# Kernel tuning notes

Hardware: AMD Instinct MI355X
Metric: run time of the kernel (lower is better)

The kernel has to match this reference:

```python
import jax, jax.numpy as jnp
import numpy as np

VX, VY = 0.2, 0.2
X_OFF = VX / 2 + 0.0          # vx/2 + pc_range[0]
Y_OFF = VY / 2 + (-40.0)      # vy/2 + pc_range[1]
K = 8                          # hardcoded in GCNLayer
BN_EPS = 1e-3
LRELU_SLOPE = 0.2
V, T, C_IN, C_OUT = 4096, 100, 4, 64


def _gcn_layer(x, conv_w, bn_gamma, bn_beta, bn_mean, bn_var):
    """DGCNN EdgeConv layer. x: [N, T, C]. Returns [N, T, O]."""
    N, Tn, C = x.shape
    # KNN on negative squared distance (self included in topk, as in torch code)
    xx = jnp.sum(x * x, axis=-1)                       # [N, T]
    inner = jnp.einsum('ntc,nsc->nts', x, x)           # [N, T, T]
    neg_dist = 2.0 * inner - xx[:, :, None] - xx[:, None, :]
    _, idx = jax.lax.top_k(neg_dist, K)                # [N, T, K]
    # gather neighbor features: nbr[n,t,k,c] = x[n, idx[n,t,k], c]
    nbr = x[jnp.arange(N)[:, None, None], idx]         # [N, T, K, C]
    xc = x[:, :, None, :]                              # [N, T, 1, C]
    edge = jnp.concatenate(
        [nbr - xc, jnp.broadcast_to(xc, (N, Tn, K, C))], axis=-1)  # [N,T,K,2C]
    # 1x1 conv (no bias) + eval-mode BatchNorm + LeakyReLU(0.2)
    h = jnp.einsum('ntkc,oc->ntko', edge, conv_w)      # [N, T, K, O]
    scale = bn_gamma / jnp.sqrt(bn_var + BN_EPS)
    h = (h - bn_mean) * scale + bn_beta
    h = jax.nn.leaky_relu(h, LRELU_SLOPE)
    return jnp.max(h, axis=2)                          # max over k -> [N, T, O]


def setup_inputs() -> dict:
    key = jax.random.key(0)
    k1, k2, k3, k4, k5, k6 = jax.random.split(key, 6)
    features = jax.random.normal(k1, (V, T, C_IN), dtype=jnp.float32)
    num_voxels = jnp.maximum(
        jax.random.randint(k2, (V,), 0, T), 1).astype(jnp.int32)
    coors = jax.random.randint(k3, (V, 4), 0, 352).astype(jnp.int32)
    # GCNLayer params: Conv2d(18, 64, 1, bias=False) + BatchNorm2d(64)
    conv_w = jax.random.normal(k4, (C_OUT, 18), dtype=jnp.float32) * 0.1
    bn_gamma = jnp.ones((C_OUT,), jnp.float32)
    bn_beta = jnp.zeros((C_OUT,), jnp.float32)
    bn_mean = jax.random.normal(k5, (C_OUT,), jnp.float32) * 0.1
    bn_var = 1.0 + 0.1 * jax.random.uniform(k6, (C_OUT,), jnp.float32)
    return {"features": features, "conv_w": conv_w, "bn_gamma": bn_gamma,
            "bn_beta": bn_beta, "bn_mean": bn_mean, "bn_var": bn_var,
            "num_voxels": num_voxels, "coors": coors}


def reference(features, conv_w, bn_gamma, bn_beta, bn_mean, bn_var,
              num_voxels, coors):
    nv = num_voxels.astype(features.dtype)
    # decorate: cluster offsets (xyz - mean) and pillar-center offsets (xy)
    points_mean = jnp.sum(features[:, :, :3], axis=1, keepdims=True) / nv[:, None, None]
    f_cluster = features[:, :, :3] - points_mean                      # [V,T,3]
    fx = features[:, :, 0] - (coors[:, 3].astype(features.dtype)[:, None] * VX + X_OFF)
    fy = features[:, :, 1] - (coors[:, 2].astype(features.dtype)[:, None] * VY + Y_OFF)
    f_center = jnp.stack([fx, fy], axis=-1)                           # [V,T,2]
    feat = jnp.concatenate([features, f_cluster, f_center], axis=-1)  # [V,T,9]
    # padding mask: point t valid iff t < num_voxels[v]
    mask = (jnp.arange(T)[None, :] < num_voxels[:, None]).astype(features.dtype)
    feat = feat * mask[:, :, None]
    # single GCN (last) layer; batch_process chunking is a no-op mathematically
    out = _gcn_layer(feat, conv_w, bn_gamma, bn_beta, bn_mean, bn_var)  # [V,T,64]
    out = out * mask[:, :, None]            # (+ zeros prev_features_out)
    out = jnp.max(out, axis=1)              # max over points -> [V, 64]
    return out
```

## Files before the change

kernel.cpp:

```cpp
#include <hip/hip_runtime.h>

#define TPTS 100
#define CO   64
#define KK   8

__device__ __forceinline__ unsigned umin_(unsigned a, unsigned b) { return a < b ? a : b; }
__device__ __forceinline__ unsigned umax_(unsigned a, unsigned b) { return a > b ? a : b; }

__device__ __forceinline__ unsigned dist_key(const float4 qt, const float4 qs, unsigned s) {
    float dx = qt.x - qs.x, dy = qt.y - qs.y;
    float dz = qt.z - qs.z, dw = qt.w - qs.w;
    float e = __fmaf_rn(dx, dx, __fmaf_rn(dy, dy, __fmaf_rn(dz, dz, dw * dw)));
    return (__float_as_uint(e) & 0xFFFFFF80u) | s;
}

__device__ __forceinline__ void ins8(unsigned val[KK], unsigned key) {
    #pragma unroll
    for (int k = KK - 1; k >= 1; --k)
        val[k] = umin_(val[k], umax_(val[k - 1], key));
    val[0] = umin_(val[0], key);
}

__global__ __launch_bounds__(256) void dgcnn_kernel(
    const float* __restrict__ features,
    const float* __restrict__ conv_w,
    const float* __restrict__ bn_gamma,
    const float* __restrict__ bn_beta,
    const float* __restrict__ bn_mean,
    const float* __restrict__ bn_var,
    const int*  __restrict__ num_voxels,
    const int*  __restrict__ coors,
    float* __restrict__ out)
{
    __shared__ float    s_feat[TPTS][12];
    __shared__ float    s_xx[TPTS];
    __shared__ unsigned s_idxp[TPTS][2];
    __shared__ float    s_red[4][CO];
    __shared__ float    s_mean[4];
    __shared__ union {
        float stage[TPTS][4];
        float g[TPTS][CO];
    } s_u;

    const float INF = __builtin_inff();
    const int v   = blockIdx.x;
    const int tid = threadIdx.x;
    const int nv  = num_voxels[v];

    float4 f = make_float4(0.f, 0.f, 0.f, 0.f);
    if (tid < TPTS) {
        f = reinterpret_cast<const float4*>(features)[v * TPTS + tid];
        *reinterpret_cast<float4*>(&s_u.stage[tid][0]) = f;
    }
    __syncthreads();

    if (tid < 96) {
        int ch = tid >> 5, j = tid & 31;
        float p = s_u.stage[j][ch] + s_u.stage[j + 32][ch] + s_u.stage[j + 64][ch];
        if (j < 4) p += s_u.stage[j + 96][ch];
        #pragma unroll
        for (int off = 16; off >= 1; off >>= 1)
            p += __shfl_xor(p, off, 32);
        if (j == 0) s_mean[ch] = p / (float)nv;
    }
    __syncthreads();

    if (tid < TPTS) {
        float mask = (tid < nv) ? 1.0f : 0.0f;
        float c3 = (float)coors[v * 4 + 3];
        float c2 = (float)coors[v * 4 + 2];
        float r0 = f.x * mask, r1 = f.y * mask, r2 = f.z * mask, r3 = f.w * mask;
        float r4 = (f.x - s_mean[0]) * mask;
        float r5 = (f.y - s_mean[1]) * mask;
        float r6 = (f.z - s_mean[2]) * mask;
        float r7 = (f.x - (c3 * 0.2f + 0.1f)) * mask;
        float r8 = (f.y - (c2 * 0.2f - 39.9f)) * mask;
        float xx = r0*r0 + r1*r1 + r2*r2 + r3*r3 + r4*r4
                 + r5*r5 + r6*r6 + r7*r7 + r8*r8;
        float4* rowv = reinterpret_cast<float4*>(&s_feat[tid][0]);
        rowv[0] = make_float4(1.7320508075688772f * r0,
                              1.7320508075688772f * r1,
                              1.4142135623730951f * r2, r3);
        rowv[1] = make_float4(r4, r5, r6, r7);
        rowv[2] = make_float4(r8, 0.f, 0.f, 0.f);
        s_xx[tid] = xx;
    }

    const int o  = tid & 63;
    const int wv = tid >> 6;
    const float sgn = (bn_gamma[o] < 0.f) ? -1.f : 1.f;
    float w1[9], w2[9];
    #pragma unroll
    for (int c = 0; c < 9; ++c) {
        const float ws = (c == 0 || c == 1) ? 0.57735026918962576f
                       : (c == 2) ? 0.70710678118654752f : 1.f;
        float a = conv_w[o * 18 + c];
        float b = conv_w[o * 18 + 9 + c];
        w1[c] = a * sgn * ws;
        w2[c] = (b - a) * sgn * ws;
    }
    __syncthreads();

    if (wv * 32 < nv) {
        const int trow = wv * 32 + (o & 31);
        const int bsd  = o >> 5;
        if (trow < nv) {
            const float4 qt = *reinterpret_cast<const float4*>(&s_feat[trow][0]);
            unsigned val[KK];
            #pragma unroll
            for (int k = 0; k < KK; ++k) val[k] = 0xFFFFFFFFu;
            const int h  = (nv + 1) >> 1;
            int s        = bsd ? h  : 0;
            const int se = bsd ? nv : h;
            #pragma unroll 2
            for (; s < se; ++s) {
                const float4 qs = *reinterpret_cast<const float4*>(&s_feat[s][0]);
                ins8(val, dist_key(qt, qs, (unsigned)s));
            }
            if (bsd) {
                int mcnt = TPTS - nv; if (mcnt > KK) mcnt = KK;
                unsigned kmb = __float_as_uint(s_xx[trow]) & 0xFFFFFF80u;
                for (int j = 0; j < mcnt; ++j)
                    ins8(val, kmb | (unsigned)(nv + j));
            }
            unsigned other[KK];
            #pragma unroll
            for (int k = 0; k < KK; ++k) other[k] = __shfl_xor(val[k], 32);
            if (!bsd) {
                unsigned m[KK];
                #pragma unroll
                for (int k = 0; k < KK; ++k)
                    m[k] = umin_(val[k], other[KK - 1 - k]) & 127u;
                unsigned p0 = m[0] | (m[1] << 8) | (m[2] << 16) | (m[3] << 24);
                unsigned p1 = m[4] | (m[5] << 8) | (m[6] << 16) | (m[7] << 24);
                *reinterpret_cast<uint2*>(&s_idxp[trow][0]) = make_uint2(p0, p1);
            }
        }
    }

    {
        int r0 = nv + wv, r1 = nv + wv + 4;
        if (r0 < TPTS) s_u.g[r0][o] = 0.f;
        if (r1 < TPTS) s_u.g[r1][o] = 0.f;
    }

    for (int sR = wv; sR < nv; sR += 4) {
        const float4* row = reinterpret_cast<const float4*>(&s_feat[sR][0]);
        float4 a = row[0], b = row[1];
        float c8 = s_feat[sR][8];
        float g = a.x * w1[0];
        g = __fmaf_rn(a.y, w1[1], g);
        g = __fmaf_rn(a.z, w1[2], g);
        g = __fmaf_rn(a.w, w1[3], g);
        g = __fmaf_rn(b.x, w1[4], g);
        g = __fmaf_rn(b.y, w1[5], g);
        g = __fmaf_rn(b.z, w1[6], g);
        g = __fmaf_rn(b.w, w1[7], g);
        g = __fmaf_rn(c8,  w1[8], g);
        s_u.g[sR][o] = g;
    }
    __syncthreads();

    float acc = -INF;
    for (int tt = wv; tt < nv; tt += 4) {
        const float4* row = reinterpret_cast<const float4*>(&s_feat[tt][0]);
        float4 a = row[0], b = row[1];
        float c8 = s_feat[tt][8];
        float base = a.x * w2[0];
        base = __fmaf_rn(a.y, w2[1], base);
        base = __fmaf_rn(a.z, w2[2], base);
        base = __fmaf_rn(a.w, w2[3], base);
        base = __fmaf_rn(b.x, w2[4], base);
        base = __fmaf_rn(b.y, w2[5], base);
        base = __fmaf_rn(b.z, w2[6], base);
        base = __fmaf_rn(b.w, w2[7], base);
        base = __fmaf_rn(c8,  w2[8], base);
        uint2 pk = *reinterpret_cast<const uint2*>(&s_idxp[tt][0]);
        int i0 =  pk.x        & 255, i1 = (pk.x >>  8) & 255;
        int i2 = (pk.x >> 16) & 255, i3 = (pk.x >> 24) & 255;
        int i4 =  pk.y        & 255, i5 = (pk.y >>  8) & 255;
        int i6 = (pk.y >> 16) & 255, i7 = (pk.y >> 24) & 255;
        float g0 = s_u.g[i0][o], g1 = s_u.g[i1][o], g2 = s_u.g[i2][o], g3 = s_u.g[i3][o];
        float g4 = s_u.g[i4][o], g5 = s_u.g[i5][o], g6 = s_u.g[i6][o], g7 = s_u.g[i7][o];
        float gm = fmaxf(fmaxf(fmaxf(g0, g1), fmaxf(g2, g3)),
                         fmaxf(fmaxf(g4, g5), fmaxf(g6, g7)));
        acc = fmaxf(acc, gm + base);
    }
    s_red[wv][o] = acc;
    __syncthreads();

    if (tid < CO) {
        float m = fmaxf(fmaxf(s_red[0][tid], s_red[1][tid]),
                        fmaxf(s_red[2][tid], s_red[3][tid]));
        float scale = bn_gamma[tid] / sqrtf(bn_var[tid] + 0.001f);
        float bias  = bn_beta[tid] - bn_mean[tid] * scale;
        float h = m * fabsf(scale) + bias;
        float a = (h > 0.f) ? h : 0.2f * h;
        if (nv < TPTS) a = fmaxf(a, 0.f);
        out[v * CO + tid] = a;
    }
}

extern "C" void kernel_launch(void* const* d_in, const int* in_sizes, int n_in,
                              void* d_out, int out_size, void* d_ws, size_t ws_size,
                              hipStream_t stream) {
    const float* features = (const float*)d_in[0];
    const float* conv_w   = (const float*)d_in[1];
    const float* bn_gamma = (const float*)d_in[2];
    const float* bn_beta  = (const float*)d_in[3];
    const float* bn_mean  = (const float*)d_in[4];
    const float* bn_var   = (const float*)d_in[5];
    const int*   num_vox  = (const int*)d_in[6];
    const int*   coor     = (const int*)d_in[7];
    float* outp = (float*)d_out;
    const int V = in_sizes[6];
    dgcnn_kernel<<<V, 256, 0, stream>>>(features, conv_w, bn_gamma, bn_beta,
                                        bn_mean, bn_var, num_vox, coor, outp);
}
```

Before: 118.8 us.

## Use med3 insertion, fp16 gather table, balanced KNN split, idle-wave projection

Replaces the min/max pair in the top-8 insertion network with a single v_med3_u32 instruction. Stores the per-point projected table g in fp16 instead of fp32, halving LDS use for the gather table. Rebalances the two-half KNN split to account for the padded-entry insertions, and assigns the projection loop to waves that are idle during KNN when few points are valid. The fp16 storage reduces precision of the intermediate activations, which may introduce small output errors.

```diff
diff --git a/kernel.cpp b/kernel.cpp
--- a/kernel.cpp
+++ b/kernel.cpp
@@ -6,6 +6,12 @@
 
 __device__ __forceinline__ unsigned umin_(unsigned a, unsigned b) { return a < b ? a : b; }
 __device__ __forceinline__ unsigned umax_(unsigned a, unsigned b) { return a > b ? a : b; }
+
+__device__ __forceinline__ unsigned med3u(unsigned a, unsigned b, unsigned c) {
+    unsigned d;
+    asm("v_med3_u32 %0, %1, %2, %3" : "=v"(d) : "v"(a), "v"(b), "v"(c));
+    return d;
+}
 
 __device__ __forceinline__ unsigned dist_key(const float4 qt, const float4 qs, unsigned s) {
     float dx = qt.x - qs.x, dy = qt.y - qs.y;
@@ -17,7 +23,7 @@
 __device__ __forceinline__ void ins8(unsigned val[KK], unsigned key) {
     #pragma unroll
     for (int k = KK - 1; k >= 1; --k)
-        val[k] = umin_(val[k], umax_(val[k - 1], key));
+        val[k] = med3u(val[k - 1], val[k], key);
     val[0] = umin_(val[0], key);
 }
 
@@ -38,8 +44,8 @@
     __shared__ float    s_red[4][CO];
     __shared__ float    s_mean[4];
     __shared__ union {
-        float stage[TPTS][4];
-        float g[TPTS][CO];
+        float    stage[TPTS][4];
+        _Float16 g16[TPTS][CO];
     } s_u;
 
     const float INF = __builtin_inff();
@@ -101,7 +107,9 @@
     }
     __syncthreads();
 
-    if (wv * 32 < nv) {
+    const int nd = (nv + 31) >> 5;
+
+    if (wv < nd) {
         const int trow = wv * 32 + (o & 31);
         const int bsd  = o >> 5;
         if (trow < nv) {
@@ -109,16 +117,16 @@
             unsigned val[KK];
             #pragma unroll
             for (int k = 0; k < KK; ++k) val[k] = 0xFFFFFFFFu;
-            const int h  = (nv + 1) >> 1;
-            int s        = bsd ? h  : 0;
-            const int se = bsd ? nv : h;
+            int mcnt = TPTS - nv; if (mcnt > KK) mcnt = KK;
+            int ha = (nv + mcnt + 1) >> 1; if (ha > nv) ha = nv;
+            int s        = bsd ? ha : 0;
+            const int se = bsd ? nv : ha;
             #pragma unroll 2
             for (; s < se; ++s) {
                 const float4 qs = *reinterpret_cast<const float4*>(&s_feat[s][0]);
                 ins8(val, dist_key(qt, qs, (unsigned)s));
             }
             if (bsd) {
-                int mcnt = TPTS - nv; if (mcnt > KK) mcnt = KK;
                 unsigned kmb = __float_as_uint(s_xx[trow]) & 0xFFFFFF80u;
                 for (int j = 0; j < mcnt; ++j)
                     ins8(val, kmb | (unsigned)(nv + j));
@@ -140,24 +148,29 @@
 
     {
         int r0 = nv + wv, r1 = nv + wv + 4;
-        if (r0 < TPTS) s_u.g[r0][o] = 0.f;
-        if (r1 < TPTS) s_u.g[r1][o] = 0.f;
-    }
-
-    for (int sR = wv; sR < nv; sR += 4) {
-        const float4* row = reinterpret_cast<const float4*>(&s_feat[sR][0]);
-        float4 a = row[0], b = row[1];
-        float c8 = s_feat[sR][8];
-        float g = a.x * w1[0];
-        g = __fmaf_rn(a.y, w1[1], g);
-        g = __fmaf_rn(a.z, w1[2], g);
-        g = __fmaf_rn(a.w, w1[3], g);
-        g = __fmaf_rn(b.x, w1[4], g);
-        g = __fmaf_rn(b.y, w1[5], g);
-        g = __fmaf_rn(b.z, w1[6], g);
-        g = __fmaf_rn(b.w, w1[7], g);
-        g = __fmaf_rn(c8,  w1[8], g);
-        s_u.g[sR][o] = g;
+        if (r0 < TPTS) s_u.g16[r0][o] = (_Float16)0.f;
+        if (r1 < TPTS) s_u.g16[r1][o] = (_Float16)0.f;
+    }
+
+    {
+        int sR, step;
+        if (nd <= 2) { sR = (wv >= nd) ? (wv - nd) : nv; step = 4 - nd; }
+        else         { sR = wv;                          step = 4;      }
+        for (; sR < nv; sR += step) {
+            const float4* row = reinterpret_cast<const float4*>(&s_feat[sR][0]);
+            float4 a = row[0], b = row[1];
+            float c8 = s_feat[sR][8];
+            float g = a.x * w1[0];
+            g = __fmaf_rn(a.y, w1[1], g);
+            g = __fmaf_rn(a.z, w1[2], g);
+            g = __fmaf_rn(a.w, w1[3], g);
+            g = __fmaf_rn(b.x, w1[4], g);
+            g = __fmaf_rn(b.y, w1[5], g);
+            g = __fmaf_rn(b.z, w1[6], g);
+            g = __fmaf_rn(b.w, w1[7], g);
+            g = __fmaf_rn(c8,  w1[8], g);
+            s_u.g16[sR][o] = (_Float16)g;
+        }
     }
     __syncthreads();
 
@@ -180,8 +193,10 @@
         int i2 = (pk.x >> 16) & 255, i3 = (pk.x >> 24) & 255;
         int i4 =  pk.y        & 255, i5 = (pk.y >>  8) & 255;
         int i6 = (pk.y >> 16) & 255, i7 = (pk.y >> 24) & 255;
-        float g0 = s_u.g[i0][o], g1 = s_u.g[i1][o], g2 = s_u.g[i2][o], g3 = s_u.g[i3][o];
-        float g4 = s_u.g[i4][o], g5 = s_u.g[i5][o], g6 = s_u.g[i6][o], g7 = s_u.g[i7][o];
+        float g0 = (float)s_u.g16[i0][o], g1 = (float)s_u.g16[i1][o];
+        float g2 = (float)s_u.g16[i2][o], g3 = (float)s_u.g16[i3][o];
+        float g4 = (float)s_u.g16[i4][o], g5 = (float)s_u.g16[i5][o];
+        float g6 = (float)s_u.g16[i6][o], g7 = (float)s_u.g16[i7][o];
         float gm = fmaxf(fmaxf(fmaxf(g0, g1), fmaxf(g2, g3)),
                          fmaxf(fmaxf(g4, g5), fmaxf(g6, g7)));
         acc = fmaxf(acc, gm + base);
```

Result: faster. 111.0 us (-6.5%).
